# Kernel optimization log

Hardware: AMD Instinct MI355X
Metric: run time of the kernel (lower is better)

## Reference

```python
import math
import jax, jax.numpy as jnp
import numpy as np

# Frozen random shifts from the original module's __init__ (random.randint(-1,1))
SHIFT_C = 1   # p_2_0_1: roll along channel dim
SHIFT_H = 1   # p_4_1_0: roll along h
SHIFT_W = -1  # p_4_1_1: roll along w
K = 7         # horizontal window size (F.unfold kernel (1,7), padding (0,3))


def setup_inputs() -> dict:
    key = jax.random.key(0)
    k1, k2 = jax.random.split(key)
    n, c, h, w = 8, 256, 56, 56
    x = jax.random.normal(k1, (n, c, h, w), dtype=jnp.float32)
    # p_1_w ~ trunc_normal(std=0.1) around 1.0; approximate with 1 + 0.1*normal
    p1w = 1.0 + 0.1 * jax.random.normal(k2, (1, c, h, w), dtype=jnp.float32)
    return {"x": x, "p1w": p1w}


def _unfold_w7(t):
    # t: (n,c,h,w) -> (n,c,7,h,w): 7 horizontal taps, zero-padded (pad=3)
    w = t.shape[-1]
    tp = jnp.pad(t, ((0, 0), (0, 0), (0, 0), (3, 3)))
    return jnp.stack([tp[..., j:j + w] for j in range(K)], axis=2)


def reference(x, p1w):
    n, c, h, w = x.shape
    hw = h * w
    t1 = p1w * x                              # (n,c,h,w)
    t2 = jnp.roll(t1, SHIFT_C, axis=1)        # roll channels
    t3 = _unfold_w7(t2)                       # (n,c,7,h,w)
    t4 = jnp.roll(jnp.roll(t3, SHIFT_H, axis=3), SHIFT_W, axis=4)
    t5 = t1[:, :, None] - t3                  # (n,c,7,h,w)
    t6 = x[:, :, None] + t4                   # (n,c,7,h,w)
    x2 = x.reshape(n, c, hw)
    t5r = t5.reshape(n, c, K, hw)
    t6r = t6.reshape(n, c, K, hw)
    # scores: bmm(x (n,c,hw), t5^T (n,hw,c*7)) -> (n,c,c,7)
    t7 = jnp.einsum('nip,njkp->nijk', x2, t5r) / math.sqrt(hw)
    # aggregate: bmm(t7 (n,c,c*7), t6 (n,c*7,hw)) -> (n,c,hw)
    t8 = jnp.einsum('nijk,njkp->nip', t7, t6r) / math.sqrt(c * K)
    return t8.reshape(n, c, h, w)
```

## Files before the change

### kernel.cpp

```cpp
#include <hip/hip_runtime.h>

typedef unsigned short u16;
typedef __bf16 bf16x8 __attribute__((ext_vector_type(8)));
typedef float f32x4 __attribute__((ext_vector_type(4)));

#define HH  56
#define WW  56
#define HW  3136
#define CC  256
#define NB  8
#define CKP 2048
#define KS1 4

__device__ __forceinline__ u16 f2bf(float f) {
  unsigned int u = __float_as_uint(f);
  u += 0x7fffu + ((u >> 16) & 1u);
  return (u16)(u >> 16);
}
__device__ __forceinline__ float bf2f(u16 v) {
  return __uint_as_float((unsigned)v << 16);
}

__device__ __forceinline__ void lds_load16(const void* g, void* l) {
  __builtin_amdgcn_global_load_lds(
      (const __attribute__((address_space(1))) void*)g,
      (__attribute__((address_space(3))) void*)l, 16, 0, 0);
}

__global__ void pass1(const float* __restrict__ x, const float* __restrict__ p1w,
                      u16* __restrict__ t1b, u16* __restrict__ xb) {
  int i = blockIdx.x * 256 + threadIdx.x;
  int cw = i % (CC * HW / 4);
  float4 xv = ((const float4*)x)[i];
  float4 wv = ((const float4*)p1w)[cw];
  uint2 xo = make_uint2((unsigned)f2bf(xv.x) | ((unsigned)f2bf(xv.y) << 16),
                        (unsigned)f2bf(xv.z) | ((unsigned)f2bf(xv.w) << 16));
  ((uint2*)xb)[i] = xo;
  uint2 to = make_uint2((unsigned)f2bf(xv.x * wv.x) | ((unsigned)f2bf(xv.y * wv.y) << 16),
                        (unsigned)f2bf(xv.z * wv.z) | ((unsigned)f2bf(xv.w * wv.w) << 16));
  ((uint2*)t1b)[i] = to;
}

__global__ __launch_bounds__(256)
void gemm1f(const u16* __restrict__ A, const u16* __restrict__ t1b,
            float* __restrict__ Cp) {
  __shared__ u16 As[128 * 64];
  __shared__ u16 Bs[128 * 64];

  const int z = blockIdx.z, nb = z / KS1, ks = z % KS1;
  const int it0 = 49 * ks / KS1, it1 = 49 * (ks + 1) / KS1;
  const u16* Ab  = A   + (long)nb * CC * HW;
  const u16* t1n = t1b + (long)nb * CC * HW;
  const int m0 = blockIdx.x * 128, n0 = blockIdx.y * 128;
  const int jb = blockIdx.y * 16;
  const int t = threadIdx.x;
  const int lane = t & 63, wave = t >> 6;
  const int wm = wave & 1, wn = wave >> 1;
  const int lm = lane & 15, quad = lane >> 4;

  const int jl = (t >> 3) & 15, pc = t & 7, hf = t >> 7;
  const int j  = jb + jl;
  const int jm = (j + CC - 1) & (CC - 1);
  const u16* arow = t1n + (long)j  * HW;
  const u16* wrow = t1n + (long)jm * HW;

  f32x4 acc[4][4];
#pragma unroll
  for (int a = 0; a < 4; ++a)
#pragma unroll
    for (int b = 0; b < 4; ++b) acc[a][b] = (f32x4)0.0f;

  int rowc[4], colc[4];
#pragma unroll
  for (int ci = 0; ci < 4; ++ci) {
    int c = t + ci * 256;
    rowc[ci] = c >> 3;
    colc[ci] = ((c & 7) ^ (rowc[ci] & 7)) * 8;
  }

  for (int it = it0; it < it1; ++it) {
    const int k0 = it * 64;
#pragma unroll
    for (int ci = 0; ci < 4; ++ci)
      lds_load16(Ab + (long)(m0 + rowc[ci]) * HW + k0 + colc[ci],
                 &As[(t + ci * 256) * 8]);

    {
      const int p8 = k0 + pc * 8;
      u16 Ar[8], Wd[24];
      *(uint4*)Ar = *(const uint4*)&arow[p8];
#pragma unroll
      for (int L = 0; L < 3; ++L) {
        int ad = p8 - 8 + L * 8;
        ad = ad < 0 ? 0 : (ad > HW - 8 ? HW - 8 : ad);
        *(uint4*)&Wd[L * 8] = *(const uint4*)&wrow[ad];
      }
      int w0t = p8 % 56;
      float Af[8];
#pragma unroll
      for (int e = 0; e < 8; ++e) Af[e] = bf2f(Ar[e]);
      if (hf == 0) {
#pragma unroll
        for (int k = 0; k < 4; ++k) {
          u16 v[8];
#pragma unroll
          for (int e = 0; e < 8; ++e) {
            int w = w0t + e; if (w >= 56) w -= 56;
            float tap = ((unsigned)(w + k - 3) < 56u) ? bf2f(Wd[e + k + 5]) : 0.f;
            v[e] = f2bf(Af[e] - tap);
          }
          *(uint4*)&Bs[(jl * 8 + k) * 64 + (pc ^ k) * 8] = make_uint4(
              v[0] | ((unsigned)v[1] << 16), v[2] | ((unsigned)v[3] << 16),
              v[4] | ((unsigned)v[5] << 16), v[6] | ((unsigned)v[7] << 16));
        }
      } else {
#pragma unroll
        for (int k = 4; k < 7; ++k) {
          u16 v[8];
#pragma unroll
          for (int e = 0; e < 8; ++e) {
            int w = w0t + e; if (w >= 56) w -= 56;
            float tap = ((unsigned)(w + k - 3) < 56u) ? bf2f(Wd[e + k + 5]) : 0.f;
            v[e] = f2bf(Af[e] - tap);
          }
          *(uint4*)&Bs[(jl * 8 + k) * 64 + (pc ^ k) * 8] = make_uint4(
              v[0] | ((unsigned)v[1] << 16), v[2] | ((unsigned)v[3] << 16),
              v[4] | ((unsigned)v[5] << 16), v[6] | ((unsigned)v[7] << 16));
        }
        *(uint4*)&Bs[(jl * 8 + 7) * 64 + (pc ^ 7) * 8] = make_uint4(0, 0, 0, 0);
      }
    }
    __syncthreads();
#pragma unroll
    for (int kk = 0; kk < 2; ++kk) {
      const int phys = ((kk * 4 + quad) ^ (lm & 7)) * 8;
      bf16x8 af[4], bv[4];
#pragma unroll
      for (int mi = 0; mi < 4; ++mi)
        af[mi] = *(const bf16x8*)&As[(wm * 64 + mi * 16 + lm) * 64 + phys];
#pragma unroll
      for (int ni = 0; ni < 4; ++ni)
        bv[ni] = *(const bf16x8*)&Bs[(wn * 64 + ni * 16 + lm) * 64 + phys];
#pragma unroll
      for (int mi = 0; mi < 4; ++mi)
#pragma unroll
        for (int ni = 0; ni < 4; ++ni)
          acc[mi][ni] = __builtin_amdgcn_mfma_f32_16x16x32_bf16(
              af[mi], bv[ni], acc[mi][ni], 0, 0, 0);
    }
    __syncthreads();
  }

  float* Cb = Cp + ((long)ks * NB + nb) * (long)CC * CKP;
#pragma unroll
  for (int mi = 0; mi < 4; ++mi)
#pragma unroll
    for (int ni = 0; ni < 4; ++ni) {
      int rb = m0 + wm * 64 + mi * 16 + quad * 4;
      int cg = n0 + wn * 64 + ni * 16 + lm;
#pragma unroll
      for (int r = 0; r < 4; ++r)
        Cb[(long)(rb + r) * CKP + cg] = acc[mi][ni][r];
    }
}

__global__ void reduce1(const float* __restrict__ p1, u16* __restrict__ t7) {
  const int i = blockIdx.x * 256 + threadIdx.x;
  const long S = (long)NB * CC * CKP / 4;
  float4 a = ((const float4*)p1)[i];
  float4 b = ((const float4*)p1)[i + S];
  float4 c = ((const float4*)p1)[i + 2 * S];
  float4 d = ((const float4*)p1)[i + 3 * S];
  const float s = 1.0f / 56.0f;
  float e0 = (a.x + b.x + c.x + d.x) * s;
  float e1 = (a.y + b.y + c.y + d.y) * s;
  float e2 = (a.z + b.z + c.z + d.z) * s;
  float e3 = (a.w + b.w + c.w + d.w) * s;
  u16 w3 = (i & 1) ? (u16)0 : f2bf(e3);
  ushort4 o = make_ushort4(f2bf(e0), f2bf(e1), f2bf(e2), w3);
  ((ushort4*)t7)[i] = o;
}

__global__ __launch_bounds__(256)
void gemm2f(const u16* __restrict__ A, const float* __restrict__ x,
            const u16* __restrict__ t1b, float* __restrict__ out) {
  __shared__ u16 As[128 * 64];
  __shared__ u16 Bs[64 * 64];

  const int nb = blockIdx.z;
  const u16* Ab   = A   + (long)nb * CC * CKP;
  const float* xn = x   + (long)nb * CC * HW;
  const u16* t1n  = t1b + (long)nb * CC * HW;
  const int m0 = blockIdx.x * 128, n0 = blockIdx.y * 64;
  const int t = threadIdx.x;
  const int lane = t & 63, wave = t >> 6;
  const int wm = wave & 1, wn = wave >> 1;
  const int lm = lane & 15, quad = lane >> 4;

  const int pr = t & 63, jg = t >> 6;
  const int p  = n0 + pr;
  const int h  = p / WW, w = p - h * WW;
  const int h2 = (h + HH - 1) % HH;
  const int w2 = (w + 1) % WW;
  const int swz = pr & 7;

  f32x4 acc[4][2];
#pragma unroll
  for (int a = 0; a < 4; ++a)
#pragma unroll
    for (int b = 0; b < 2; ++b) acc[a][b] = (f32x4)0.0f;

  int rowc[4], colc[4];
#pragma unroll
  for (int ci = 0; ci < 4; ++ci) {
    int c = t + ci * 256;
    rowc[ci] = c >> 3;
    colc[ci] = ((c & 7) ^ (rowc[ci] & 7)) * 8;
  }

  for (int it = 0; it < 32; ++it) {
    const int k0 = it * 64;
#pragma unroll
    for (int ci = 0; ci < 4; ++ci)
      lds_load16(Ab + (long)(m0 + rowc[ci]) * CKP + k0 + colc[ci],
                 &As[(t + ci * 256) * 8]);

#pragma unroll
    for (int jj = 0; jj < 2; ++jj) {
      const int jch = it * 8 + jg * 2 + jj;
      const int jmm = (jch + CC - 1) & (CC - 1);
      const float xv = xn[(long)jch * HW + p];
      const u16* trow = t1n + (long)jmm * HW + h2 * WW;
      u16 v[8];
#pragma unroll
      for (int k = 0; k < 7; ++k) {
        int ww = w2 + k - 3;
        int wc = ww < 0 ? 0 : (ww > 55 ? 55 : ww);
        float tv = bf2f(trow[wc]);
        float tap = ((unsigned)ww < 56u) ? tv : 0.f;
        v[k] = f2bf(xv + tap);
      }
      v[7] = 0;
      *(uint4*)&Bs[pr * 64 + (((jg * 2 + jj) ^ swz) * 8)] = make_uint4(
          v[0] | ((unsigned)v[1] << 16), v[2] | ((unsigned)v[3] << 16),
          v[4] | ((unsigned)v[5] << 16), v[6] | ((unsigned)v[7] << 16));
    }
    __syncthreads();
#pragma unroll
    for (int kk = 0; kk < 2; ++kk) {
      const int phys = ((kk * 4 + quad) ^ (lm & 7)) * 8;
      bf16x8 af[4], bv[2];
#pragma unroll
      for (int mi = 0; mi < 4; ++mi)
        af[mi] = *(const bf16x8*)&As[(wm * 64 + mi * 16 + lm) * 64 + phys];
#pragma unroll
      for (int ni = 0; ni < 2; ++ni)
        bv[ni] = *(const bf16x8*)&Bs[(wn * 32 + ni * 16 + lm) * 64 + phys];
#pragma unroll
      for (int mi = 0; mi < 4; ++mi)
#pragma unroll
        for (int ni = 0; ni < 2; ++ni)
          acc[mi][ni] = __builtin_amdgcn_mfma_f32_16x16x32_bf16(
              af[mi], bv[ni], acc[mi][ni], 0, 0, 0);
    }
    __syncthreads();
  }

  const float s2 = 0.023622783f;
  float* Ob = out + (long)nb * CC * HW;
#pragma unroll
  for (int mi = 0; mi < 4; ++mi)
#pragma unroll
    for (int ni = 0; ni < 2; ++ni) {
      int rb = m0 + wm * 64 + mi * 16 + quad * 4;
      int cg = n0 + wn * 32 + ni * 16 + lm;
#pragma unroll
      for (int r = 0; r < 4; ++r)
        Ob[(long)(rb + r) * HW + cg] = acc[mi][ni][r] * s2;
    }
}

extern "C" void kernel_launch(void* const* d_in, const int* in_sizes, int n_in,
                              void* d_out, int out_size, void* d_ws, size_t ws_size,
                              hipStream_t stream) {
  const float* x   = (const float*)d_in[0];
  const float* p1w = (const float*)d_in[1];

  char* ws = (char*)d_ws;
  size_t o = 0;
  u16* xb  = (u16*)(ws + o); o += (size_t)NB * CC * HW * 2;
  u16* t1b = (u16*)(ws + o); o += (size_t)NB * CC * HW * 2;
  u16* t7  = (u16*)(ws + o); o += (size_t)NB * CC * CKP * 2;
  float* p1 = (float*)(ws + o); o += (size_t)KS1 * NB * CC * CKP * 4;

  pass1<<<NB * CC * HW / 4 / 256, 256, 0, stream>>>(x, p1w, t1b, xb);
  gemm1f<<<dim3(2, 16, NB * KS1), 256, 0, stream>>>(xb, t1b, p1);
  reduce1<<<NB * CC * CKP / 4 / 256, 256, 0, stream>>>(p1, t7);
  gemm2f<<<dim3(2, 49, NB), 256, 0, stream>>>(t7, x, t1b, (float*)d_out);
}
```

Before: 210.2 us.

## Double-buffer LDS tiles in both GEMMs and halve gemm1 split-K

Both GEMM kernels now keep two LDS buffers. The next A tile is staged with async global-to-LDS loads, and the next B tile is generated after the MFMA work on the current buffer, so there is one barrier per iteration instead of two. The split-K factor for the first GEMM drops from 4 to 2, which halves the partial-sum traffic and the reduce reads at the cost of fewer blocks. gemm2 also reads bf16 x from the workspace instead of fp32 x. The doubled LDS footprint may reduce occupancy.

```diff
diff --git a/kernel.cpp b/kernel.cpp
--- a/kernel.cpp
+++ b/kernel.cpp
@@ -10,7 +10,7 @@
 #define CC  256
 #define NB  8
 #define CKP 2048
-#define KS1 4
+#define KS1 2
 
 __device__ __forceinline__ u16 f2bf(float f) {
   unsigned int u = __float_as_uint(f);
@@ -44,8 +44,8 @@
 __global__ __launch_bounds__(256)
 void gemm1f(const u16* __restrict__ A, const u16* __restrict__ t1b,
             float* __restrict__ Cp) {
-  __shared__ u16 As[128 * 64];
-  __shared__ u16 Bs[128 * 64];
+  __shared__ u16 As[2 * 8192];
+  __shared__ u16 Bs[2 * 8192];
 
   const int z = blockIdx.z, nb = z / KS1, ks = z % KS1;
   const int it0 = 49 * ks / KS1, it1 = 49 * (ks + 1) / KS1;
@@ -78,69 +78,80 @@
     colc[ci] = ((c & 7) ^ (rowc[ci] & 7)) * 8;
   }
 
-  for (int it = it0; it < it1; ++it) {
+  auto stageA = [&](int it, int buf) {
     const int k0 = it * 64;
 #pragma unroll
     for (int ci = 0; ci < 4; ++ci)
       lds_load16(Ab + (long)(m0 + rowc[ci]) * HW + k0 + colc[ci],
-                 &As[(t + ci * 256) * 8]);
-
-    {
-      const int p8 = k0 + pc * 8;
-      u16 Ar[8], Wd[24];
-      *(uint4*)Ar = *(const uint4*)&arow[p8];
-#pragma unroll
-      for (int L = 0; L < 3; ++L) {
-        int ad = p8 - 8 + L * 8;
-        ad = ad < 0 ? 0 : (ad > HW - 8 ? HW - 8 : ad);
-        *(uint4*)&Wd[L * 8] = *(const uint4*)&wrow[ad];
+                 &As[buf * 8192 + (t + ci * 256) * 8]);
+  };
+
+  auto genB = [&](int it, int buf) {
+    const int k0 = it * 64;
+    const int p8 = k0 + pc * 8;
+    u16* Bp = &Bs[buf * 8192];
+    u16 Ar[8], Wd[24];
+    *(uint4*)Ar = *(const uint4*)&arow[p8];
+#pragma unroll
+    for (int L = 0; L < 3; ++L) {
+      int ad = p8 - 8 + L * 8;
+      ad = ad < 0 ? 0 : (ad > HW - 8 ? HW - 8 : ad);
+      *(uint4*)&Wd[L * 8] = *(const uint4*)&wrow[ad];
+    }
+    int w0t = p8 % 56;
+    float Af[8];
+#pragma unroll
+    for (int e = 0; e < 8; ++e) Af[e] = bf2f(Ar[e]);
+    if (hf == 0) {
+#pragma unroll
+      for (int k = 0; k < 4; ++k) {
+        u16 v[8];
+#pragma unroll
+        for (int e = 0; e < 8; ++e) {
+          int w = w0t + e; if (w >= 56) w -= 56;
+          float tap = ((unsigned)(w + k - 3) < 56u) ? bf2f(Wd[e + k + 5]) : 0.f;
+          v[e] = f2bf(Af[e] - tap);
+        }
+        *(uint4*)&Bp[(jl * 8 + k) * 64 + (pc ^ k) * 8] = make_uint4(
+            v[0] | ((unsigned)v[1] << 16), v[2] | ((unsigned)v[3] << 16),
+            v[4] | ((unsigned)v[5] << 16), v[6] | ((unsigned)v[7] << 16));
       }
-      int w0t = p8 % 56;
-      float Af[8];
-#pragma unroll
-      for (int e = 0; e < 8; ++e) Af[e] = bf2f(Ar[e]);
-      if (hf == 0) {
-#pragma unroll
-        for (int k = 0; k < 4; ++k) {
-          u16 v[8];
-#pragma unroll
-          for (int e = 0; e < 8; ++e) {
-            int w = w0t + e; if (w >= 56) w -= 56;
-            float tap = ((unsigned)(w + k - 3) < 56u) ? bf2f(Wd[e + k + 5]) : 0.f;
-            v[e] = f2bf(Af[e] - tap);
-          }
-          *(uint4*)&Bs[(jl * 8 + k) * 64 + (pc ^ k) * 8] = make_uint4(
-              v[0] | ((unsigned)v[1] << 16), v[2] | ((unsigned)v[3] << 16),
-              v[4] | ((unsigned)v[5] << 16), v[6] | ((unsigned)v[7] << 16));
+    } else {
+#pragma unroll
+      for (int k = 4; k < 7; ++k) {
+        u16 v[8];
+#pragma unroll
+        for (int e = 0; e < 8; ++e) {
+          int w = w0t + e; if (w >= 56) w -= 56;
+          float tap = ((unsigned)(w + k - 3) < 56u) ? bf2f(Wd[e + k + 5]) : 0.f;
+          v[e] = f2bf(Af[e] - tap);
         }
-      } else {
-#pragma unroll
-        for (int k = 4; k < 7; ++k) {
-          u16 v[8];
-#pragma unroll
-          for (int e = 0; e < 8; ++e) {
-            int w = w0t + e; if (w >= 56) w -= 56;
-            float tap = ((unsigned)(w + k - 3) < 56u) ? bf2f(Wd[e + k + 5]) : 0.f;
-            v[e] = f2bf(Af[e] - tap);
-          }
-          *(uint4*)&Bs[(jl * 8 + k) * 64 + (pc ^ k) * 8] = make_uint4(
-              v[0] | ((unsigned)v[1] << 16), v[2] | ((unsigned)v[3] << 16),
-              v[4] | ((unsigned)v[5] << 16), v[6] | ((unsigned)v[7] << 16));
-        }
-        *(uint4*)&Bs[(jl * 8 + 7) * 64 + (pc ^ 7) * 8] = make_uint4(0, 0, 0, 0);
+        *(uint4*)&Bp[(jl * 8 + k) * 64 + (pc ^ k) * 8] = make_uint4(
+            v[0] | ((unsigned)v[1] << 16), v[2] | ((unsigned)v[3] << 16),
+            v[4] | ((unsigned)v[5] << 16), v[6] | ((unsigned)v[7] << 16));
       }
-    }
-    __syncthreads();
+      *(uint4*)&Bp[(jl * 8 + 7) * 64 + (pc ^ 7) * 8] = make_uint4(0, 0, 0, 0);
+    }
+  };
+
+  stageA(it0, 0);
+  genB(it0, 0);
+  __syncthreads();
+
+  for (int it = it0; it < it1; ++it) {
+    const int cb = (it - it0) & 1;
+    const int itn = it + 1 < it1 ? it + 1 : it;
+    stageA(itn, cb ^ 1);
 #pragma unroll
     for (int kk = 0; kk < 2; ++kk) {
       const int phys = ((kk * 4 + quad) ^ (lm & 7)) * 8;
       bf16x8 af[4], bv[4];
 #pragma unroll
       for (int mi = 0; mi < 4; ++mi)
-        af[mi] = *(const bf16x8*)&As[(wm * 64 + mi * 16 + lm) * 64 + phys];
+        af[mi] = *(const bf16x8*)&As[cb * 8192 + (wm * 64 + mi * 16 + lm) * 64 + phys];
 #pragma unroll
       for (int ni = 0; ni < 4; ++ni)
-        bv[ni] = *(const bf16x8*)&Bs[(wn * 64 + ni * 16 + lm) * 64 + phys];
+        bv[ni] = *(const bf16x8*)&Bs[cb * 8192 + (wn * 64 + ni * 16 + lm) * 64 + phys];
 #pragma unroll
       for (int mi = 0; mi < 4; ++mi)
 #pragma unroll
@@ -148,6 +159,7 @@
           acc[mi][ni] = __builtin_amdgcn_mfma_f32_16x16x32_bf16(
               af[mi], bv[ni], acc[mi][ni], 0, 0, 0);
     }
+    genB(itn, cb ^ 1);
     __syncthreads();
   }
 
@@ -169,28 +181,26 @@
   const long S = (long)NB * CC * CKP / 4;
   float4 a = ((const float4*)p1)[i];
   float4 b = ((const float4*)p1)[i + S];
-  float4 c = ((const float4*)p1)[i + 2 * S];
-  float4 d = ((const float4*)p1)[i + 3 * S];
   const float s = 1.0f / 56.0f;
-  float e0 = (a.x + b.x + c.x + d.x) * s;
-  float e1 = (a.y + b.y + c.y + d.y) * s;
-  float e2 = (a.z + b.z + c.z + d.z) * s;
-  float e3 = (a.w + b.w + c.w + d.w) * s;
+  float e0 = (a.x + b.x) * s;
+  float e1 = (a.y + b.y) * s;
+  float e2 = (a.z + b.z) * s;
+  float e3 = (a.w + b.w) * s;
   u16 w3 = (i & 1) ? (u16)0 : f2bf(e3);
   ushort4 o = make_ushort4(f2bf(e0), f2bf(e1), f2bf(e2), w3);
   ((ushort4*)t7)[i] = o;
 }
 
 __global__ __launch_bounds__(256)
-void gemm2f(const u16* __restrict__ A, const float* __restrict__ x,
+void gemm2f(const u16* __restrict__ A, const u16* __restrict__ xb,
             const u16* __restrict__ t1b, float* __restrict__ out) {
-  __shared__ u16 As[128 * 64];
-  __shared__ u16 Bs[64 * 64];
+  __shared__ u16 As[2 * 8192];
+  __shared__ u16 Bs[2 * 4096];
 
   const int nb = blockIdx.z;
-  const u16* Ab   = A   + (long)nb * CC * CKP;
-  const float* xn = x   + (long)nb * CC * HW;
-  const u16* t1n  = t1b + (long)nb * CC * HW;
+  const u16* Ab  = A   + (long)nb * CC * CKP;
+  const u16* xbn = xb  + (long)nb * CC * HW;
+  const u16* t1n = t1b + (long)nb * CC * HW;
   const int m0 = blockIdx.x * 128, n0 = blockIdx.y * 64;
   const int t = threadIdx.x;
   const int lane = t & 63, wave = t >> 6;
@@ -218,18 +228,21 @@
     colc[ci] = ((c & 7) ^ (rowc[ci] & 7)) * 8;
   }
 
-  for (int it = 0; it < 32; ++it) {
+  auto stageA = [&](int it, int buf) {
     const int k0 = it * 64;
 #pragma unroll
     for (int ci = 0; ci < 4; ++ci)
       lds_load16(Ab + (long)(m0 + rowc[ci]) * CKP + k0 + colc[ci],
-                 &As[(t + ci * 256) * 8]);
-
+                 &As[buf * 8192 + (t + ci * 256) * 8]);
+  };
+
+  auto genB = [&](int it, int buf) {
+    u16* Bp = &Bs[buf * 4096];
 #pragma unroll
     for (int jj = 0; jj < 2; ++jj) {
       const int jch = it * 8 + jg * 2 + jj;
       const int jmm = (jch + CC - 1) & (CC - 1);
-      const float xv = xn[(long)jch * HW + p];
+      const float xv = bf2f(xbn[(long)jch * HW + p]);
       const u16* trow = t1n + (long)jmm * HW + h2 * WW;
       u16 v[8];
 #pragma unroll
@@ -241,21 +254,30 @@
         v[k] = f2bf(xv + tap);
       }
       v[7] = 0;
-      *(uint4*)&Bs[pr * 64 + (((jg * 2 + jj) ^ swz) * 8)] = make_uint4(
+      *(uint4*)&Bp[pr * 64 + (((jg * 2 + jj) ^ swz) * 8)] = make_uint4(
           v[0] | ((unsigned)v[1] << 16), v[2] | ((unsigned)v[3] << 16),
           v[4] | ((unsigned)v[5] << 16), v[6] | ((unsigned)v[7] << 16));
     }
-    __syncthreads();
+  };
+
+  stageA(0, 0);
+  genB(0, 0);
+  __syncthreads();
+
+  for (int it = 0; it < 32; ++it) {
+    const int cb = it & 1;
+    const int itn = it + 1 < 32 ? it + 1 : it;
+    stageA(itn, cb ^ 1);
 #pragma unroll
     for (int kk = 0; kk < 2; ++kk) {
       const int phys = ((kk * 4 + quad) ^ (lm & 7)) * 8;
       bf16x8 af[4], bv[2];
 #pragma unroll
       for (int mi = 0; mi < 4; ++mi)
-        af[mi] = *(const bf16x8*)&As[(wm * 64 + mi * 16 + lm) * 64 + phys];
+        af[mi] = *(const bf16x8*)&As[cb * 8192 + (wm * 64 + mi * 16 + lm) * 64 + phys];
 #pragma unroll
       for (int ni = 0; ni < 2; ++ni)
-        bv[ni] = *(const bf16x8*)&Bs[(wn * 32 + ni * 16 + lm) * 64 + phys];
+        bv[ni] = *(const bf16x8*)&Bs[cb * 4096 + (wn * 32 + ni * 16 + lm) * 64 + phys];
 #pragma unroll
       for (int mi = 0; mi < 4; ++mi)
 #pragma unroll
@@ -263,6 +285,7 @@
           acc[mi][ni] = __builtin_amdgcn_mfma_f32_16x16x32_bf16(
               af[mi], bv[ni], acc[mi][ni], 0, 0, 0);
     }
+    genB(itn, cb ^ 1);
     __syncthreads();
   }
 
@@ -296,5 +319,5 @@
   pass1<<<NB * CC * HW / 4 / 256, 256, 0, stream>>>(x, p1w, t1b, xb);
   gemm1f<<<dim3(2, 16, NB * KS1), 256, 0, stream>>>(xb, t1b, p1);
   reduce1<<<NB * CC * CKP / 4 / 256, 256, 0, stream>>>(p1, t7);
-  gemm2f<<<dim3(2, 49, NB), 256, 0, stream>>>(t7, x, t1b, (float*)d_out);
-}
+  gemm2f<<<dim3(2, 49, NB), 256, 0, stream>>>(t7, xb, t1b, (float*)d_out);
+}
```

After: 234.8 us. 1.12x slower.
